# Kernel tuning notes

Measured on AMD Instinct MI355X. Metric: run time of the kernel, lower is better.

Reference implementation:

```python
import jax, jax.numpy as jnp
import numpy as np

K = 501   # box-filter length (conv kernel height)
P = 250   # reflect padding on each side of the time axis


def setup_inputs() -> dict:
    key = jax.random.key(0)
    k1, k2 = jax.random.split(key)
    pred = jax.random.normal(k1, (8, 16384, 128), dtype=jnp.float32)  # [B, T, C]
    # Conv2d default bias init: U(-b, b) with b = 1/sqrt(fan_in) = 1/sqrt(501)
    b = 1.0 / np.sqrt(K)
    bias = jax.random.uniform(k2, (1,), dtype=jnp.float32, minval=-b, maxval=b)
    return {"pred": pred, "bias": bias}


def reference(pred, bias):
    # Reflect-pad the time axis, then compute the 501-wide moving sum via a
    # prefix-sum (O(N) instead of O(N*K) dense conv) — same math as the
    # all-ones Conv2d kernel with reflect padding.
    x = jnp.pad(pred, ((0, 0), (P, P), (0, 0)), mode="reflect")  # [B, T+2P, C]
    c = jnp.cumsum(x, axis=1)
    c = jnp.concatenate([jnp.zeros_like(c[:, :1, :]), c], axis=1)  # [B, T+2P+1, C]
    win_sum = c[:, K:, :] - c[:, :-K, :]                            # [B, T, C]
    smoothed = (win_sum + bias[0]) / K  # conv output (ones weights + bias) / kernel_size
    return jnp.maximum(pred, smoothed)
```

## Files before the change

kernel.cpp:

```cpp
#include <hip/hip_runtime.h>


constexpr int B    = 8;
constexpr int T    = 16384;
constexpr int C    = 128;
constexpr int K    = 501;
constexpr int CHN  = 16;
constexpr int NCG  = C / CHN;
constexpr int NSEG = 32;
constexpr int SEGR = T / NSEG;

__device__ __forceinline__ int ridx(int j) {
    j = (j < 0) ? -j : j;
    return (j >= T) ? (2 * T - 2 - j) : j;
}

__global__ __launch_bounds__(64, 4) void smoother_kernel(
    const float* __restrict__ pred, const float* __restrict__ bias,
    float* __restrict__ out) {
    const int b   = blockIdx.x & 7;
    const int cg  = (blockIdx.x >> 3) & 7;
    const int seg = blockIdx.x >> 6;
    const int g0  = seg * SEGR;

    const int lane = threadIdx.x & 63;
    const int q    = lane >> 4;
    const int ch   = lane & 15;

    const float* pb = pred + (size_t)b * T * C + cg * CHN + ch;
    float*       ob = out  + (size_t)b * T * C + cg * CHN + ch;

    const float rk  = 1.0f / (float)K;
    const float brk = bias[0] * rk;

    const bool interior = (g0 >= 251) && (g0 + SEGR + 251 <= T);

    float acc = 0.0f;
    if (interior) {
        #pragma unroll 5
        for (int i = 0; i < 125; ++i)
            acc += pb[(g0 - 250 + 4 * i + q) * C];
    } else {
        #pragma unroll 5
        for (int i = 0; i < 125; ++i)
            acc += pb[ridx(g0 - 250 + 4 * i + q) * C];
    }
    float a2 = acc + __shfl_xor(acc, 16);
    float S  = a2 + __shfl_xor(a2, 32);
    S += pb[(interior ? (g0 + 250) : ridx(g0 + 250)) * C];

    int tn = g0 + 251 + q;
    int to = g0 - 250 + q;
    int tc = g0 + q;
    const int srcl = 48 + ch;

    if (interior) {
        #pragma unroll 8
        for (int i = 0; i < SEGR / 4; ++i) {
            const float vn = pb[tn * C];
            const float vo = pb[to * C];
            const float vc = pb[tc * C];
            const float d  = vn - vo;
            float x = d;
            const float u1 = __shfl_up(x, 16); if (lane >= 16) x += u1;
            const float u2 = __shfl_up(x, 32); if (lane >= 32) x += u2;
            const float tot = __shfl(x, srcl);
            const float sm  = S + (x - d);
            const float o   = fmaxf(vc, fmaf(sm, rk, brk));
            __builtin_nontemporal_store(o, &ob[tc * C]);
            S += tot;
            tn += 4; to += 4; tc += 4;
        }
    } else {
        #pragma unroll 4
        for (int i = 0; i < SEGR / 4; ++i) {
            const float vn = pb[ridx(tn) * C];
            const float vo = pb[ridx(to) * C];
            const float vc = pb[tc * C];
            const float d  = vn - vo;
            float x = d;
            const float u1 = __shfl_up(x, 16); if (lane >= 16) x += u1;
            const float u2 = __shfl_up(x, 32); if (lane >= 32) x += u2;
            const float tot = __shfl(x, srcl);
            const float sm  = S + (x - d);
            const float o   = fmaxf(vc, fmaf(sm, rk, brk));
            __builtin_nontemporal_store(o, &ob[tc * C]);
            S += tot;
            tn += 4; to += 4; tc += 4;
        }
    }
}

extern "C" void kernel_launch(void* const* d_in, const int* in_sizes, int n_in,
                              void* d_out, int out_size, void* d_ws, size_t ws_size,
                              hipStream_t stream) {
    const float* pred = (const float*)d_in[0];
    const float* bias = (const float*)d_in[1];
    float*       out  = (float*)d_out;

    const int blocks = B * NCG * NSEG;
    smoother_kernel<<<blocks, 64, 0, stream>>>(pred, bias, out);
}
```

Baseline: 146.6 us.

## Stage input rows in an LDS ring buffer and read windows from shared memory

Result: faster. 132.8 us (-9.4%).

```diff
diff --git a/kernel.cpp b/kernel.cpp
--- a/kernel.cpp
+++ b/kernel.cpp
@@ -1,93 +1,127 @@
 #include <hip/hip_runtime.h>
 
 
-constexpr int B    = 8;
-constexpr int T    = 16384;
-constexpr int C    = 128;
-constexpr int K    = 501;
-constexpr int CHN  = 16;
-constexpr int NCG  = C / CHN;
-constexpr int NSEG = 32;
-constexpr int SEGR = T / NSEG;
+constexpr int B     = 8;
+constexpr int T     = 16384;
+constexpr int C     = 128;
+constexpr int K     = 501;
+constexpr int CHN   = 16;
+constexpr int NCG   = C / CHN;
+constexpr int NSEG  = 16;
+constexpr int SEGR  = T / NSEG;
+constexpr int CHK   = 32;
+constexpr int RROWS = 576;
+constexpr int RPAD  = 17;
+constexpr int RSZ   = RROWS * RPAD;
+constexpr int MARG  = 256;
+constexpr int PRO   = 17;
+constexpr int NCHK  = 48;
 
 __device__ __forceinline__ int ridx(int j) {
     j = (j < 0) ? -j : j;
     return (j >= T) ? (2 * T - 2 - j) : j;
 }
 
-__global__ __launch_bounds__(64, 4) void smoother_kernel(
+__global__ __launch_bounds__(256, 4) void smoother_kernel(
     const float* __restrict__ pred, const float* __restrict__ bias,
     float* __restrict__ out) {
+    __shared__ float ring[RSZ];
+
     const int b   = blockIdx.x & 7;
     const int cg  = (blockIdx.x >> 3) & 7;
     const int seg = blockIdx.x >> 6;
     const int g0  = seg * SEGR;
+    const int jstart = g0 - MARG;
 
-    const int lane = threadIdx.x & 63;
-    const int q    = lane >> 4;
-    const int ch   = lane & 15;
+    const int tid  = threadIdx.x;
+    const int lane = tid & 63;
+    const int w    = tid >> 6;
+    const int rowq = lane >> 2;
+    const int cs   = lane & 3;
+    const int ch   = w * 4 + cs;
 
-    const float* pb = pred + (size_t)b * T * C + cg * CHN + ch;
-    float*       ob = out  + (size_t)b * T * C + cg * CHN + ch;
+    const int srow = tid >> 3;
+    const int chp  = tid & 7;
+
+    const float* pb = pred + (size_t)b * T * C + cg * CHN;
+    float*       ob = out  + (size_t)b * T * C + cg * CHN;
 
     const float rk  = 1.0f / (float)K;
     const float brk = bias[0] * rk;
 
-    const bool interior = (g0 >= 251) && (g0 + SEGR + 251 <= T);
+    {
+        float2 pv0[PRO];
+        #pragma unroll
+        for (int m = 0; m < PRO; ++m) {
+            const int jr = ridx(jstart + m * CHK + srow);
+            pv0[m] = *reinterpret_cast<const float2*>(
+                pb + (size_t)jr * C + chp * 2);
+        }
+        #pragma unroll
+        for (int m = 0; m < PRO; ++m) {
+            const int p = m * CHK + srow;
+            float* d = &ring[p * RPAD + chp * 2];
+            d[0] = pv0[m].x; d[1] = pv0[m].y;
+        }
+    }
+    __syncthreads();
 
     float acc = 0.0f;
-    if (interior) {
-        #pragma unroll 5
-        for (int i = 0; i < 125; ++i)
-            acc += pb[(g0 - 250 + 4 * i + q) * C];
-    } else {
-        #pragma unroll 5
-        for (int i = 0; i < 125; ++i)
-            acc += pb[ridx(g0 - 250 + 4 * i + q) * C];
-    }
-    float a2 = acc + __shfl_xor(acc, 16);
-    float S  = a2 + __shfl_xor(a2, 32);
-    S += pb[(interior ? (g0 + 250) : ridx(g0 + 250)) * C];
+    #pragma unroll 8
+    for (int k2 = 0; k2 < 31; ++k2)
+        acc += ring[(6 + rowq + 16 * k2) * RPAD + ch];
+    if (rowq <= 4) acc += ring[(502 + rowq) * RPAD + ch];
+    acc += __shfl_xor(acc, 4);
+    acc += __shfl_xor(acc, 8);
+    acc += __shfl_xor(acc, 16);
+    acc += __shfl_xor(acc, 32);
+    float S = acc;
 
-    int tn = g0 + 251 + q;
-    int to = g0 - 250 + q;
-    int tc = g0 + q;
-    const int srcl = 48 + ch;
+    int idxn = (507 + rowq) * RPAD + ch;
+    int idxo = (6   + rowq) * RPAD + ch;
+    int idxc = (256 + rowq) * RPAD + ch;
+    float* op = ob + (size_t)(g0 + rowq) * C + ch;
 
-    if (interior) {
-        #pragma unroll 8
-        for (int i = 0; i < SEGR / 4; ++i) {
-            const float vn = pb[tn * C];
-            const float vo = pb[to * C];
-            const float vc = pb[tc * C];
+    int pm = PRO * CHK;
+    float2 pv;
+
+    for (int i = 0; i < SEGR / CHK; ++i) {
+        const bool do_stage = (i + PRO) < NCHK;
+        if (do_stage) {
+            const int jr = ridx(jstart + (i + PRO) * CHK + srow);
+            pv = *reinterpret_cast<const float2*>(
+                pb + (size_t)jr * C + chp * 2);
+        }
+
+        #pragma unroll
+        for (int s = 0; s < 2; ++s) {
+            const float vn = ring[idxn];
+            const float vo = ring[idxo];
+            const float vc = ring[idxc];
             const float d  = vn - vo;
             float x = d;
-            const float u1 = __shfl_up(x, 16); if (lane >= 16) x += u1;
-            const float u2 = __shfl_up(x, 32); if (lane >= 32) x += u2;
-            const float tot = __shfl(x, srcl);
+            const float u1 = __shfl_up(x, 4);  if (lane >= 4)  x += u1;
+            const float u2 = __shfl_up(x, 8);  if (lane >= 8)  x += u2;
+            const float u3 = __shfl_up(x, 16); if (lane >= 16) x += u3;
+            const float u4 = __shfl_up(x, 32); if (lane >= 32) x += u4;
+            const float tot = __shfl(x, 60 + cs);
             const float sm  = S + (x - d);
             const float o   = fmaxf(vc, fmaf(sm, rk, brk));
-            __builtin_nontemporal_store(o, &ob[tc * C]);
+            __builtin_nontemporal_store(o, op);
             S += tot;
-            tn += 4; to += 4; tc += 4;
+            idxn += 16 * RPAD; if (idxn >= RSZ) idxn -= RSZ;
+            idxo += 16 * RPAD; if (idxo >= RSZ) idxo -= RSZ;
+            idxc += 16 * RPAD; if (idxc >= RSZ) idxc -= RSZ;
+            op += 16 * C;
         }
-    } else {
-        #pragma unroll 4
-        for (int i = 0; i < SEGR / 4; ++i) {
-            const float vn = pb[ridx(tn) * C];
-            const float vo = pb[ridx(to) * C];
-            const float vc = pb[tc * C];
-            const float d  = vn - vo;
-            float x = d;
-            const float u1 = __shfl_up(x, 16); if (lane >= 16) x += u1;
-            const float u2 = __shfl_up(x, 32); if (lane >= 32) x += u2;
-            const float tot = __shfl(x, srcl);
-            const float sm  = S + (x - d);
-            const float o   = fmaxf(vc, fmaf(sm, rk, brk));
-            __builtin_nontemporal_store(o, &ob[tc * C]);
-            S += tot;
-            tn += 4; to += 4; tc += 4;
+
+        if (do_stage) {
+            int p = pm + srow; if (p >= RROWS) p -= RROWS;
+            float* d = &ring[p * RPAD + chp * 2];
+            d[0] = pv.x; d[1] = pv.y;
+            pm += CHK; if (pm >= RROWS) pm -= RROWS;
         }
+        __syncthreads();
     }
 }
 
@@ -99,5 +133,5 @@
     float*       out  = (float*)d_out;
 
     const int blocks = B * NCG * NSEG;
-    smoother_kernel<<<blocks, 64, 0, stream>>>(pred, bias, out);
+    smoother_kernel<<<blocks, 256, 0, stream>>>(pred, bias, out);
 }
```

## Vectorize smoother with float4 per lane and 8-row wave scan

Applied to the files above, without the earlier changes.

After: 129.9 us. 1.13x faster.

```diff
diff --git a/kernel.cpp b/kernel.cpp
--- a/kernel.cpp
+++ b/kernel.cpp
@@ -5,88 +5,128 @@
 constexpr int T    = 16384;
 constexpr int C    = 128;
 constexpr int K    = 501;
-constexpr int CHN  = 16;
+constexpr int CHN  = 32;
 constexpr int NCG  = C / CHN;
-constexpr int NSEG = 32;
+constexpr int NSEG = 64;
 constexpr int SEGR = T / NSEG;
+constexpr int RPR  = C / 4;
+
+typedef float f32x4 __attribute__((ext_vector_type(4)));
 
 __device__ __forceinline__ int ridx(int j) {
     j = (j < 0) ? -j : j;
     return (j >= T) ? (2 * T - 2 - j) : j;
 }
 
-__global__ __launch_bounds__(64, 4) void smoother_kernel(
+__device__ __forceinline__ float4 shfl_up4(const float4 v, int d) {
+    float4 r;
+    r.x = __shfl_up(v.x, d); r.y = __shfl_up(v.y, d);
+    r.z = __shfl_up(v.z, d); r.w = __shfl_up(v.w, d);
+    return r;
+}
+__device__ __forceinline__ float4 shfl_xor4(const float4 v, int m) {
+    float4 r;
+    r.x = __shfl_xor(v.x, m); r.y = __shfl_xor(v.y, m);
+    r.z = __shfl_xor(v.z, m); r.w = __shfl_xor(v.w, m);
+    return r;
+}
+__device__ __forceinline__ float4 shfl4(const float4 v, int src) {
+    float4 r;
+    r.x = __shfl(v.x, src); r.y = __shfl(v.y, src);
+    r.z = __shfl(v.z, src); r.w = __shfl(v.w, src);
+    return r;
+}
+
+__global__ __launch_bounds__(64) void smoother_kernel(
     const float* __restrict__ pred, const float* __restrict__ bias,
     float* __restrict__ out) {
     const int b   = blockIdx.x & 7;
-    const int cg  = (blockIdx.x >> 3) & 7;
-    const int seg = blockIdx.x >> 6;
+    const int cg  = (blockIdx.x >> 3) & (NCG - 1);
+    const int seg = blockIdx.x >> 5;
     const int g0  = seg * SEGR;
 
     const int lane = threadIdx.x & 63;
-    const int q    = lane >> 4;
-    const int ch   = lane & 15;
+    const int rowq = lane >> 3;
+    const int cq   = lane & 7;
 
-    const float* pb = pred + (size_t)b * T * C + cg * CHN + ch;
-    float*       ob = out  + (size_t)b * T * C + cg * CHN + ch;
+    const float4* p4 = reinterpret_cast<const float4*>(
+        pred + (size_t)b * T * C + cg * CHN) + cq;
+    float4* o4 = reinterpret_cast<float4*>(
+        out + (size_t)b * T * C + cg * CHN) + cq;
 
     const float rk  = 1.0f / (float)K;
     const float brk = bias[0] * rk;
 
     const bool interior = (g0 >= 251) && (g0 + SEGR + 251 <= T);
 
-    float acc = 0.0f;
+    float4 acc = make_float4(0.f, 0.f, 0.f, 0.f);
+    const int j0 = g0 - 250 + rowq;
     if (interior) {
-        #pragma unroll 5
-        for (int i = 0; i < 125; ++i)
-            acc += pb[(g0 - 250 + 4 * i + q) * C];
+        #pragma unroll 8
+        for (int k = 0; k < 62; ++k)
+            acc += p4[(j0 + 8 * k) * RPR];
+        if (rowq <= 4) acc += p4[(j0 + 496) * RPR];
     } else {
-        #pragma unroll 5
-        for (int i = 0; i < 125; ++i)
-            acc += pb[ridx(g0 - 250 + 4 * i + q) * C];
+        #pragma unroll 8
+        for (int k = 0; k < 62; ++k)
+            acc += p4[ridx(j0 + 8 * k) * RPR];
+        if (rowq <= 4) acc += p4[ridx(j0 + 496) * RPR];
     }
-    float a2 = acc + __shfl_xor(acc, 16);
-    float S  = a2 + __shfl_xor(a2, 32);
-    S += pb[(interior ? (g0 + 250) : ridx(g0 + 250)) * C];
+    acc += shfl_xor4(acc, 8);
+    acc += shfl_xor4(acc, 16);
+    acc += shfl_xor4(acc, 32);
+    float4 S = acc;
 
-    int tn = g0 + 251 + q;
-    int to = g0 - 250 + q;
-    int tc = g0 + q;
-    const int srcl = 48 + ch;
+    int t = g0 + rowq;
+    const int bsrc = 56 + cq;
 
     if (interior) {
-        #pragma unroll 8
-        for (int i = 0; i < SEGR / 4; ++i) {
-            const float vn = pb[tn * C];
-            const float vo = pb[to * C];
-            const float vc = pb[tc * C];
-            const float d  = vn - vo;
-            float x = d;
-            const float u1 = __shfl_up(x, 16); if (lane >= 16) x += u1;
-            const float u2 = __shfl_up(x, 32); if (lane >= 32) x += u2;
-            const float tot = __shfl(x, srcl);
-            const float sm  = S + (x - d);
-            const float o   = fmaxf(vc, fmaf(sm, rk, brk));
-            __builtin_nontemporal_store(o, &ob[tc * C]);
-            S += tot;
-            tn += 4; to += 4; tc += 4;
+        #pragma unroll 4
+        for (int s = 0; s < SEGR / 8; ++s) {
+            const float4 vn = p4[(t + 251) * RPR];
+            const float4 vo = p4[(t - 250) * RPR];
+            const float4 vc = p4[t * RPR];
+            float4 d = vn;
+            d.x -= vo.x; d.y -= vo.y; d.z -= vo.z; d.w -= vo.w;
+            float4 x = d;
+            float4 u;
+            u = shfl_up4(x, 8);  if (lane >= 8)  { x.x += u.x; x.y += u.y; x.z += u.z; x.w += u.w; }
+            u = shfl_up4(x, 16); if (lane >= 16) { x.x += u.x; x.y += u.y; x.z += u.z; x.w += u.w; }
+            u = shfl_up4(x, 32); if (lane >= 32) { x.x += u.x; x.y += u.y; x.z += u.z; x.w += u.w; }
+            const float4 tot = shfl4(x, bsrc);
+            float4 o;
+            o.x = fmaxf(vc.x, fmaf(S.x + (x.x - d.x), rk, brk));
+            o.y = fmaxf(vc.y, fmaf(S.y + (x.y - d.y), rk, brk));
+            o.z = fmaxf(vc.z, fmaf(S.z + (x.z - d.z), rk, brk));
+            o.w = fmaxf(vc.w, fmaf(S.w + (x.w - d.w), rk, brk));
+            __builtin_nontemporal_store(*reinterpret_cast<f32x4*>(&o),
+                                        reinterpret_cast<f32x4*>(&o4[t * RPR]));
+            S.x += tot.x; S.y += tot.y; S.z += tot.z; S.w += tot.w;
+            t += 8;
         }
     } else {
         #pragma unroll 4
-        for (int i = 0; i < SEGR / 4; ++i) {
-            const float vn = pb[ridx(tn) * C];
-            const float vo = pb[ridx(to) * C];
-            const float vc = pb[tc * C];
-            const float d  = vn - vo;
-            float x = d;
-            const float u1 = __shfl_up(x, 16); if (lane >= 16) x += u1;
-            const float u2 = __shfl_up(x, 32); if (lane >= 32) x += u2;
-            const float tot = __shfl(x, srcl);
-            const float sm  = S + (x - d);
-            const float o   = fmaxf(vc, fmaf(sm, rk, brk));
-            __builtin_nontemporal_store(o, &ob[tc * C]);
-            S += tot;
-            tn += 4; to += 4; tc += 4;
+        for (int s = 0; s < SEGR / 8; ++s) {
+            const float4 vn = p4[ridx(t + 251) * RPR];
+            const float4 vo = p4[ridx(t - 250) * RPR];
+            const float4 vc = p4[t * RPR];
+            float4 d = vn;
+            d.x -= vo.x; d.y -= vo.y; d.z -= vo.z; d.w -= vo.w;
+            float4 x = d;
+            float4 u;
+            u = shfl_up4(x, 8);  if (lane >= 8)  { x.x += u.x; x.y += u.y; x.z += u.z; x.w += u.w; }
+            u = shfl_up4(x, 16); if (lane >= 16) { x.x += u.x; x.y += u.y; x.z += u.z; x.w += u.w; }
+            u = shfl_up4(x, 32); if (lane >= 32) { x.x += u.x; x.y += u.y; x.z += u.z; x.w += u.w; }
+            const float4 tot = shfl4(x, bsrc);
+            float4 o;
+            o.x = fmaxf(vc.x, fmaf(S.x + (x.x - d.x), rk, brk));
+            o.y = fmaxf(vc.y, fmaf(S.y + (x.y - d.y), rk, brk));
+            o.z = fmaxf(vc.z, fmaf(S.z + (x.z - d.z), rk, brk));
+            o.w = fmaxf(vc.w, fmaf(S.w + (x.w - d.w), rk, brk));
+            __builtin_nontemporal_store(*reinterpret_cast<f32x4*>(&o),
+                                        reinterpret_cast<f32x4*>(&o4[t * RPR]));
+            S.x += tot.x; S.y += tot.y; S.z += tot.z; S.w += tot.w;
+            t += 8;
         }
     }
 }
```
